# Kernel optimization log

Hardware: AMD Instinct MI355X
Metric: run time of the kernel (lower is better)

## Reference

```python
import jax, jax.numpy as jnp
import numpy as np

N, D, M, E, K = 16384, 512, 1024, 8, 2
LOSS_COEF = 0.01
EPS = 1e-10


def setup_inputs() -> dict:
    key = jax.random.key(0)
    ks = jax.random.split(key, 6)
    x = jax.random.normal(ks[0], (N, D), dtype=jnp.float32)
    # gate weight (torch init is zeros; use small random so routing is non-degenerate)
    w_gate = 0.02 * jax.random.normal(ks[1], (D, E), dtype=jnp.float32)
    # stacked expert FFN params: Linear(D->M), GELU, Linear(M->D)
    W1 = jax.random.normal(ks[2], (E, D, M), dtype=jnp.float32) / np.sqrt(D)
    b1 = jnp.zeros((E, M), dtype=jnp.float32)
    W2 = jax.random.normal(ks[3], (E, M, D), dtype=jnp.float32) / np.sqrt(M)
    b2 = jnp.zeros((E, D), dtype=jnp.float32)
    return {"x": x, "w_gate": w_gate, "W1": W1, "b1": b1, "W2": W2, "b2": b2}


def _cv_squared(v):
    # torch .var() is unbiased (ddof=1)
    v = v.astype(jnp.float32)
    return jnp.var(v, ddof=1) / (jnp.mean(v) ** 2 + EPS)


def reference(x, w_gate, W1, b1, W2, b2):
    n = x.shape[0]
    # --- noisy_top_k_gating (eval path: no noise) ---
    logits = x @ w_gate                                  # [N, E]
    top_logits, top_idx = jax.lax.top_k(logits, min(K + 1, E))
    topk_logits = top_logits[:, :K]                      # [N, K]
    topk_idx = top_idx[:, :K]                            # [N, K]
    topk_gates = jax.nn.softmax(topk_logits, axis=-1)    # [N, K]
    gates = jnp.zeros_like(logits).at[jnp.arange(n)[:, None], topk_idx].set(topk_gates)
    importance = gates.sum(axis=0)                       # [E]
    load = (gates > 0).sum(axis=0).astype(jnp.float32)   # [E]
    loss = LOSS_COEF * (_cv_squared(importance) + _cv_squared(load))
    # --- experts (dense equivalent of sparse dispatch/combine: gate==0 rows contribute 0) ---
    h = jnp.einsum('nd,edm->enm', x, W1) + b1[:, None, :]     # [E, N, M]
    h = jax.nn.gelu(h, approximate=False)
    out = jnp.einsum('enm,emd->end', h, W2) + b2[:, None, :]  # [E, N, D]
    y = jnp.einsum('ne,end->nd', gates, out)                  # [N, D]
    return (y, loss)
```

## Files before the change

kernel.cpp:

```cpp
#include <hip/hip_runtime.h>
#include <math.h>

#define NTOK 16384
#define DDIM 512
#define MDIM 1024
#define NEXP 8
#define BKW 32
#define TMAX 264

typedef __attribute__((ext_vector_type(8))) short short8;
typedef __attribute__((ext_vector_type(4))) float floatx4;

__device__ inline unsigned short f2bf(float f){
  union { float f; unsigned int u; } v; v.f = f;
  unsigned int u = v.u;
  u += ((u >> 16) & 1u) + 0x7fffu;
  return (unsigned short)(u >> 16);
}

__device__ inline float bf2f(unsigned short s){
  union { unsigned int u; float f; } v;
  v.u = ((unsigned int)s) << 16;
  return v.f;
}

__device__ inline float gelu_fast(float x){
  float u = x * 0.70710678118654752f;
  float a = fabsf(u);
  float t = __builtin_amdgcn_rcpf(fmaf(0.3275911f, a, 1.0f));
  float p = fmaf(1.061405429f, t, -1.453152027f);
  p = fmaf(p, t, 1.421413741f);
  p = fmaf(p, t, -0.284496736f);
  p = fmaf(p, t, 0.254829592f);
  p = p * t;
  float e = __expf(-u * u);
  float erfa = fmaf(-p, e, 1.0f);
  float erfu = copysignf(erfa, u);
  return 0.5f * x * (1.0f + erfu);
}

__device__ __forceinline__ void gload16(const unsigned short* g, unsigned short* l){
  __builtin_amdgcn_global_load_lds(
      (const __attribute__((address_space(1))) void*)g,
      (__attribute__((address_space(3))) void*)l,
      16, 0, 0);
}


__global__ void prep_kernel(const float* __restrict__ W1, const float* __restrict__ W2,
                            unsigned short* __restrict__ w1t, unsigned short* __restrict__ w2t,
                            int* __restrict__ counts, float* __restrict__ imp,
                            int* __restrict__ rank){
  __shared__ float tile[32][33];
  int z = blockIdx.z;
  if (z == 0 && blockIdx.x == 0 && blockIdx.y == 0){
    int flat = threadIdx.y * 32 + threadIdx.x;
    if (flat < NEXP){ counts[flat] = 0; imp[flat] = 0.0f; rank[flat] = 0; }
  }
  const float* in; unsigned short* out; int R, C, c0, r0, e;
  if (z < 8){ e = z;     in = W1; out = w1t; R = DDIM; C = MDIM; c0 = blockIdx.x << 5; r0 = blockIdx.y << 5; }
  else      { e = z - 8; in = W2; out = w2t; R = MDIM; C = DDIM; c0 = blockIdx.y << 5; r0 = blockIdx.x << 5; }
  const float* src = in + (size_t)e * R * C;
  unsigned short* dst = out + (size_t)e * R * C;
  int tc = threadIdx.x;
  int tr = threadIdx.y;
  #pragma unroll
  for (int i = 0; i < 32; i += 8)
    tile[tr + i][tc] = src[(size_t)(r0 + tr + i) * C + c0 + tc];
  __syncthreads();
  #pragma unroll
  for (int i = 0; i < 32; i += 8)
    dst[(size_t)(c0 + tr + i) * R + r0 + tc] = f2bf(tile[tc][tr + i]);
}


__global__ __launch_bounds__(256)
void gating_kernel(const float* __restrict__ x,
                   const float* __restrict__ wg,
                   unsigned short* __restrict__ xb,
                   int* __restrict__ tok_e, float* __restrict__ tok_g,
                   int* __restrict__ counts, float* __restrict__ imp){
  __shared__ int   lcnt[NEXP];
  __shared__ float limp[NEXP];
  int t = threadIdx.x;
  if (t < NEXP){ lcnt[t] = 0; limp[t] = 0.0f; }
  __syncthreads();

  int wave = t >> 6;
  int lane = t & 63;

  for (int it = 0; it < 4; it++){
    int n = blockIdx.x * 16 + it * 4 + wave;

    const float4* xp = (const float4*)(x + (size_t)n * DDIM + lane * 8);
    float4 a = xp[0], b = xp[1];
    float xv[8] = {a.x, a.y, a.z, a.w, b.x, b.y, b.z, b.w};

    short8 xo;
    #pragma unroll
    for (int j = 0; j < 8; j++) xo[j] = (short)f2bf(xv[j]);
    *(short8*)(xb + (size_t)n * DDIM + lane * 8) = xo;

    double acc[NEXP];
    #pragma unroll
    for (int e = 0; e < NEXP; e++) acc[e] = 0.0;
    #pragma unroll
    for (int j = 0; j < 8; j++){
      const float* wr = wg + (size_t)(lane * 8 + j) * NEXP;
      #pragma unroll
      for (int e = 0; e < NEXP; e++) acc[e] += (double)xv[j] * (double)wr[e];
    }
    #pragma unroll
    for (int off = 32; off >= 1; off >>= 1){
      #pragma unroll
      for (int e = 0; e < NEXP; e++) acc[e] += __shfl_xor(acc[e], off);
    }
    if (lane == 0){
      int i0 = -1, i1 = -1;
      double l0 = -1e300, l1 = -1e300;
      #pragma unroll
      for (int e = 0; e < NEXP; e++){
        double v = acc[e];
        if (v > l0){ l1 = l0; i1 = i0; l0 = v; i0 = e; }
        else if (v > l1){ l1 = v; i1 = e; }
      }
      float ex = expf((float)(l1 - l0));
      float g0 = 1.0f / (1.0f + ex);
      float g1 = ex / (1.0f + ex);
      tok_e[n * 2]     = i0; tok_e[n * 2 + 1] = i1;
      tok_g[n * 2]     = g0; tok_g[n * 2 + 1] = g1;
      atomicAdd(&lcnt[i0], 1); atomicAdd(&lcnt[i1], 1);
      atomicAdd(&limp[i0], g0); atomicAdd(&limp[i1], g1);
    }
  }
  __syncthreads();
  if (t < NEXP){
    atomicAdd(&counts[t], lcnt[t]);
    atomicAdd(&imp[t], limp[t]);
  }
}


__global__ __launch_bounds__(256)
void scatter_kernel(const int* __restrict__ counts,
                    const float* __restrict__ imp,
                    const int* __restrict__ tok_e,
                    const float* __restrict__ tok_g,
                    int* __restrict__ rank,
                    int* __restrict__ offsets_g, int* __restrict__ tile_pre_g,
                    int* __restrict__ btok, int* __restrict__ slot_of,
                    float* __restrict__ out_loss){
  __shared__ int lcnt[NEXP];
  __shared__ int lbase[NEXP];
  int t = threadIdx.x;
  if (t < NEXP) lcnt[t] = 0;
  __syncthreads();

  int n = blockIdx.x * 256 + t;
  int e0 = tok_e[n * 2], e1 = tok_e[n * 2 + 1];
  int r0 = atomicAdd(&lcnt[e0], 1);
  int r1 = atomicAdd(&lcnt[e1], 1);
  __syncthreads();
  if (t < NEXP){
    int offacc = 0;
    #pragma unroll
    for (int e = 0; e < NEXP; e++){ int c = counts[e]; if (e < t) offacc += c; }
    lbase[t] = offacc + atomicAdd(&rank[t], lcnt[t]);
  }
  __syncthreads();
  int s0 = lbase[e0] + r0;
  int s1 = lbase[e1] + r1;
  btok[s0] = n;
  btok[s1] = n;
  slot_of[n * 2]     = s0;
  slot_of[n * 2 + 1] = s1;

  if (blockIdx.x == 0 && t < 64){
    int l = t;
    int   c  = (l < NEXP) ? counts[l] : 0;
    float im = (l < NEXP) ? imp[l]    : 0.0f;
    int   tl = (c + 127) >> 7;
    int poff = 0, ptl = 0, tot = 0, tott = 0;
    double si = 0, si2 = 0, sl = 0, sl2 = 0;
    #pragma unroll
    for (int e = 0; e < NEXP; e++){
      int   ce = __shfl(c, e);
      int   te = __shfl(tl, e);
      float ie = __shfl(im, e);
      if (e < l){ poff += ce; ptl += te; }
      tot += ce; tott += te;
      si += (double)ie; si2 += (double)ie * ie;
      sl += (double)ce; sl2 += (double)ce * ce;
    }
    if (l < NEXP){ offsets_g[l] = poff; tile_pre_g[l] = ptl; }
    if (l == 0){
      offsets_g[NEXP] = tot; tile_pre_g[NEXP] = tott;
      double mi = si / 8.0, ml = sl / 8.0;
      double vi = (si2 - 8.0 * mi * mi) / 7.0;
      double vl = (sl2 - 8.0 * ml * ml) / 7.0;
      *out_loss = (float)(0.01 * (vi / (mi * mi + 1e-10) + vl / (ml * ml + 1e-10)));
    }
  }
}


__global__ __launch_bounds__(512, 6)
void gemm1_kernel(const unsigned short* __restrict__ xb,
                  const unsigned short* __restrict__ w1t,
                  const float* __restrict__ b1,
                  const int* __restrict__ offsets,
                  const int* __restrict__ tile_pre,
                  const int* __restrict__ btok,
                  unsigned short* __restrict__ H){
  int b = blockIdx.x;
  int L = (b & 7) * TMAX + (b >> 3);
  int ct = L & 7;
  int tt = L >> 3;
  if (tt >= tile_pre[NEXP]) return;
  int e = 0;
  while (tt >= tile_pre[e + 1]) e++;
  int rt = tt - tile_pre[e];
  int off = offsets[e];
  int cnt = offsets[e + 1] - off;
  int r0 = rt << 7;

  __shared__ unsigned short As[3 * 128 * BKW];
  __shared__ unsigned short Bs[3 * 128 * BKW];

  int t = threadIdx.x;
  int w = t >> 6;
  int l = t & 63;
  int g = (l & 3) ^ ((l >> 3) & 3);

  const unsigned short* apt;
  {
    int ra = r0 + w * 16 + (l >> 2);  if (ra >= cnt) ra = cnt - 1;
    apt = xb + (size_t)btok[off + ra] * DDIM + g * 8;
  }
  const unsigned short* bpt = w1t + ((size_t)e * MDIM + (ct << 7) + w * 16 + (l >> 2)) * DDIM + g * 8;

  int wr = (w >> 1) << 5;
  int wc = (w & 1) << 6;
  int lm = l & 15;
  int lq = l >> 4;
  int swz = (lm >> 1) & 3;

  int aoff[2], boff[4];
  #pragma unroll
  for (int i = 0; i < 2; i++) aoff[i] = (wr + i * 16 + lm) * BKW + ((lq ^ swz) << 3);
  #pragma unroll
  for (int j = 0; j < 4; j++) boff[j] = (wc + j * 16 + lm) * BKW + ((lq ^ swz) << 3);

  floatx4 acc[2][4] = {};

  #define STAGE1(K0, CB) {                                   \
    gload16(apt + (K0), As + (CB) * 4096 + w * 512);         \
    gload16(bpt + (K0), Bs + (CB) * 4096 + w * 512);         \
  }
  #define READ1(CB) {                                        \
    const unsigned short* Ac = As + (CB) * 4096;             \
    const unsigned short* Bc = Bs + (CB) * 4096;             \
    _Pragma("unroll")                                        \
    for (int i = 0; i < 2; i++) af[i]  = *(const short8*)(Ac + aoff[i]); \
    _Pragma("unroll")                                        \
    for (int j = 0; j < 4; j++) bfr[j] = *(const short8*)(Bc + boff[j]); \
  }
  #define MFMA1 {                                            \
    _Pragma("unroll")                                        \
    for (int i = 0; i < 2; i++)                              \
      _Pragma("unroll")                                      \
      for (int j = 0; j < 4; j++)                            \
        acc[i][j] = __builtin_amdgcn_mfma_f32_16x16x32_bf16(af[i], bfr[j], acc[i][j], 0, 0, 0); \
  }
  #define WAITBAR(N) {                                       \
    asm volatile("s_waitcnt vmcnt(" #N ")" ::: "memory");    \
    __builtin_amdgcn_sched_barrier(0);                       \
    __builtin_amdgcn_s_barrier();                            \
    __builtin_amdgcn_sched_barrier(0);                       \
  }

  const int NK = DDIM / BKW;
  STAGE1(0, 0);
  STAGE1(BKW, 1);
  WAITBAR(2);
  #pragma unroll
  for (int k = 0; k < NK; k++){
    const int cur = k % 3;
    short8 af[2], bfr[4];
    READ1(cur);
    if (k < NK - 2) STAGE1((k + 2) * BKW, (k + 2) % 3);
    __builtin_amdgcn_s_setprio(1);
    MFMA1;
    __builtin_amdgcn_s_setprio(0);
    if (k < NK - 2){ WAITBAR(2); }
    else if (k == NK - 2){ WAITBAR(0); }
  }
  #undef STAGE1
  #undef READ1
  #undef MFMA1
  #undef WAITBAR

  const float* bias = b1 + e * MDIM + (ct << 7);
  #pragma unroll
  for (int i = 0; i < 2; i++){
    int rbase = wr + i * 16 + lq * 4;
    #pragma unroll
    for (int j = 0; j < 4; j++){
      int cc = wc + j * 16 + lm;
      float bv = bias[cc];
      #pragma unroll
      for (int r = 0; r < 4; r++){
        int row = r0 + rbase + r;
        if (row < cnt){
          float v = acc[i][j][r] + bv;
          H[(size_t)(off + row) * MDIM + (ct << 7) + cc] = f2bf(gelu_fast(v));
        }
      }
    }
  }
}

__global__ __launch_bounds__(512, 6)
void gemm2_kernel(const unsigned short* __restrict__ H,
                  const unsigned short* __restrict__ w2t,
                  const float* __restrict__ b2,
                  const int* __restrict__ offsets,
                  const int* __restrict__ tile_pre,
                  unsigned short* __restrict__ O){
  int b = blockIdx.x;
  int L = (b & 7) * (TMAX / 2) + (b >> 3);
  int ct = L & 3;
  int tt = L >> 2;
  if (tt >= tile_pre[NEXP]) return;
  int e = 0;
  while (tt >= tile_pre[e + 1]) e++;
  int rt = tt - tile_pre[e];
  int off = offsets[e];
  int cnt = offsets[e + 1] - off;
  int r0 = rt << 7;

  __shared__ unsigned short As[3 * 128 * BKW];
  __shared__ unsigned short Bs[3 * 128 * BKW];

  int t = threadIdx.x;
  int w = t >> 6;
  int l = t & 63;
  int g = (l & 3) ^ ((l >> 3) & 3);

  const unsigned short* apt;
  {
    int ra = r0 + w * 16 + (l >> 2);  if (ra >= cnt) ra = cnt - 1;
    apt = H + (size_t)(off + ra) * MDIM + g * 8;
  }
  const unsigned short* bpt = w2t + ((size_t)e * DDIM + (ct << 7) + w * 16 + (l >> 2)) * MDIM + g * 8;

  int wr = (w >> 1) << 5;
  int wc = (w & 1) << 6;
  int lm = l & 15;
  int lq = l >> 4;
  int swz = (lm >> 1) & 3;

  int aoff[2], boff[4];
  #pragma unroll
  for (int i = 0; i < 2; i++) aoff[i] = (wr + i * 16 + lm) * BKW + ((lq ^ swz) << 3);
  #pragma unroll
  for (int j = 0; j < 4; j++) boff[j] = (wc + j * 16 + lm) * BKW + ((lq ^ swz) << 3);

  floatx4 acc[2][4] = {};

  #define STAGE2(K0, CB) {                                   \
    gload16(apt + (K0), As + (CB) * 4096 + w * 512);         \
    gload16(bpt + (K0), Bs + (CB) * 4096 + w * 512);         \
  }
  #define READ2(CB) {                                        \
    const unsigned short* Ac = As + (CB) * 4096;             \
    const unsigned short* Bc = Bs + (CB) * 4096;             \
    _Pragma("unroll")                                        \
    for (int i = 0; i < 2; i++) af[i]  = *(const short8*)(Ac + aoff[i]); \
    _Pragma("unroll")                                        \
    for (int j = 0; j < 4; j++) bfr[j] = *(const short8*)(Bc + boff[j]); \
  }
  #define MFMA2 {                                            \
    _Pragma("unroll")                                        \
    for (int i = 0; i < 2; i++)                              \
      _Pragma("unroll")                                      \
      for (int j = 0; j < 4; j++)                            \
        acc[i][j] = __builtin_amdgcn_mfma_f32_16x16x32_bf16(af[i], bfr[j], acc[i][j], 0, 0, 0); \
  }
  #define WAITBAR2(N) {                                      \
    asm volatile("s_waitcnt vmcnt(" #N ")" ::: "memory");    \
    __builtin_amdgcn_sched_barrier(0);                       \
    __builtin_amdgcn_s_barrier();                            \
    __builtin_amdgcn_sched_barrier(0);                       \
  }

  const int NK = MDIM / BKW;
  STAGE2(0, 0);
  STAGE2(BKW, 1);
  WAITBAR2(2);
  #pragma unroll
  for (int k = 0; k < NK; k++){
    const int cur = k % 3;
    short8 af[2], bfr[4];
    READ2(cur);
    if (k < NK - 2) STAGE2((k + 2) * BKW, (k + 2) % 3);
    __builtin_amdgcn_s_setprio(1);
    MFMA2;
    __builtin_amdgcn_s_setprio(0);
    if (k < NK - 2){ WAITBAR2(2); }
    else if (k == NK - 2){ WAITBAR2(0); }
  }
  #undef STAGE2
  #undef READ2
  #undef MFMA2
  #undef WAITBAR2

  const float* bias = b2 + e * DDIM + (ct << 7);
  #pragma unroll
  for (int i = 0; i < 2; i++){
    int rbase = wr + i * 16 + lq * 4;
    #pragma unroll
    for (int j = 0; j < 4; j++){
      int cc = wc + j * 16 + lm;
      float bv = bias[cc];
      #pragma unroll
      for (int r = 0; r < 4; r++){
        int row = r0 + rbase + r;
        if (row < cnt)
          O[(size_t)(off + row) * DDIM + (ct << 7) + cc] = f2bf(acc[i][j][r] + bv);
      }
    }
  }
}


__global__ __launch_bounds__(256)
void combine_kernel(const unsigned short* __restrict__ O,
                    const float* __restrict__ tok_g,
                    const int* __restrict__ slot_of,
                    float* __restrict__ y){
  int wave = threadIdx.x >> 6;
  int lane = threadIdx.x & 63;
  int n = blockIdx.x * 4 + wave;
  int s0 = slot_of[n * 2], s1 = slot_of[n * 2 + 1];
  float g0 = tok_g[n * 2], g1 = tok_g[n * 2 + 1];
  short8 a = *(const short8*)(O + (size_t)s0 * DDIM + lane * 8);
  short8 b = *(const short8*)(O + (size_t)s1 * DDIM + lane * 8);
  float4 o0, o1;
  float* po0 = (float*)&o0;
  float* po1 = (float*)&o1;
  #pragma unroll
  for (int j = 0; j < 4; j++){
    po0[j] = g0 * bf2f((unsigned short)a[j]) + g1 * bf2f((unsigned short)b[j]);
    po1[j] = g0 * bf2f((unsigned short)a[j + 4]) + g1 * bf2f((unsigned short)b[j + 4]);
  }
  float4* yp = (float4*)(y + (size_t)n * DDIM + lane * 8);
  yp[0] = o0;
  yp[1] = o1;
}


extern "C" void kernel_launch(void* const* d_in, const int* in_sizes, int n_in,
                              void* d_out, int out_size, void* d_ws, size_t ws_size,
                              hipStream_t stream){
  const float* x  = (const float*)d_in[0];
  const float* wg = (const float*)d_in[1];
  const float* W1 = (const float*)d_in[2];
  const float* b1 = (const float*)d_in[3];
  const float* W2 = (const float*)d_in[4];
  const float* b2 = (const float*)d_in[5];
  float* y = (float*)d_out;

  char* ws = (char*)d_ws;
  size_t o = 0;
  auto alloc = [&](size_t bytes)->char*{
    char* p = ws + o;
    o += (bytes + 255) & ~(size_t)255;
    return p;
  };
  unsigned short* xb   = (unsigned short*)alloc((size_t)NTOK * DDIM * 2);
  unsigned short* w1t  = (unsigned short*)alloc((size_t)NEXP * MDIM * DDIM * 2);
  unsigned short* w2t  = (unsigned short*)alloc((size_t)NEXP * DDIM * MDIM * 2);
  unsigned short* H    = (unsigned short*)alloc((size_t)NTOK * 2 * MDIM * 2);
  unsigned short* O    = (unsigned short*)alloc((size_t)NTOK * 2 * DDIM * 2);
  int*   btok    = (int*)  alloc((size_t)NTOK * 2 * 4);
  int*   slot_of = (int*)  alloc((size_t)NTOK * 2 * 4);
  int*   tok_e   = (int*)  alloc((size_t)NTOK * 2 * 4);
  float* tok_g   = (float*)alloc((size_t)NTOK * 2 * 4);
  int*   counts  = (int*)  alloc(64);
  float* imp     = (float*)alloc(64);
  int*   rank    = (int*)  alloc(64);
  int*   offsets = (int*)  alloc(64);
  int*   tile_pre= (int*)  alloc(64);

  hipLaunchKernelGGL(prep_kernel, dim3(32, 16, 16), dim3(32, 8), 0, stream,
                     W1, W2, w1t, w2t, counts, imp, rank);
  hipLaunchKernelGGL(gating_kernel, dim3(NTOK / 16), dim3(256), 0, stream,
                     x, wg, xb, tok_e, tok_g, counts, imp);
  hipLaunchKernelGGL(scatter_kernel, dim3(NTOK / 256), dim3(256), 0, stream,
                     counts, imp, tok_e, tok_g, rank, offsets, tile_pre,
                     btok, slot_of, y + (size_t)NTOK * DDIM);
  hipLaunchKernelGGL(gemm1_kernel, dim3(TMAX * 8), dim3(512), 0, stream,
                     xb, w1t, b1, offsets, tile_pre, btok, H);
  hipLaunchKernelGGL(gemm2_kernel, dim3(TMAX * 4), dim3(512), 0, stream,
                     H, w2t, b2, offsets, tile_pre, O);
  hipLaunchKernelGGL(combine_kernel, dim3(NTOK / 4), dim3(256), 0, stream,
                     O, tok_g, slot_of, y);
}
```

Baseline: 268.3 us.

## Fuse weight prep into gating kernel and scatter GEMM2 outputs to token order

```diff
diff --git a/kernel.cpp b/kernel.cpp
--- a/kernel.cpp
+++ b/kernel.cpp
@@ -47,42 +47,39 @@
 }
 
 
-__global__ void prep_kernel(const float* __restrict__ W1, const float* __restrict__ W2,
-                            unsigned short* __restrict__ w1t, unsigned short* __restrict__ w2t,
-                            int* __restrict__ counts, float* __restrict__ imp,
-                            int* __restrict__ rank){
+__global__ __launch_bounds__(256)
+void prep_gating_kernel(const float* __restrict__ x,
+                        const float* __restrict__ wg,
+                        const float* __restrict__ W1, const float* __restrict__ W2,
+                        unsigned short* __restrict__ xb,
+                        unsigned short* __restrict__ w1t, unsigned short* __restrict__ w2t,
+                        int* __restrict__ tok_e, float* __restrict__ tok_g,
+                        int* __restrict__ counts, float* __restrict__ imp){
   __shared__ float tile[32][33];
-  int z = blockIdx.z;
-  if (z == 0 && blockIdx.x == 0 && blockIdx.y == 0){
-    int flat = threadIdx.y * 32 + threadIdx.x;
-    if (flat < NEXP){ counts[flat] = 0; imp[flat] = 0.0f; rank[flat] = 0; }
-  }
-  const float* in; unsigned short* out; int R, C, c0, r0, e;
-  if (z < 8){ e = z;     in = W1; out = w1t; R = DDIM; C = MDIM; c0 = blockIdx.x << 5; r0 = blockIdx.y << 5; }
-  else      { e = z - 8; in = W2; out = w2t; R = MDIM; C = DDIM; c0 = blockIdx.y << 5; r0 = blockIdx.x << 5; }
-  const float* src = in + (size_t)e * R * C;
-  unsigned short* dst = out + (size_t)e * R * C;
-  int tc = threadIdx.x;
-  int tr = threadIdx.y;
-  #pragma unroll
-  for (int i = 0; i < 32; i += 8)
-    tile[tr + i][tc] = src[(size_t)(r0 + tr + i) * C + c0 + tc];
-  __syncthreads();
-  #pragma unroll
-  for (int i = 0; i < 32; i += 8)
-    dst[(size_t)(c0 + tr + i) * R + r0 + tc] = f2bf(tile[tc][tr + i]);
-}
-
-
-__global__ __launch_bounds__(256)
-void gating_kernel(const float* __restrict__ x,
-                   const float* __restrict__ wg,
-                   unsigned short* __restrict__ xb,
-                   int* __restrict__ tok_e, float* __restrict__ tok_g,
-                   int* __restrict__ counts, float* __restrict__ imp){
   __shared__ int   lcnt[NEXP];
   __shared__ float limp[NEXP];
   int t = threadIdx.x;
+
+  if (blockIdx.x >= 1024){
+    int pb = blockIdx.x - 1024;
+    int bx = pb & 31, by = (pb >> 5) & 15, z = pb >> 9;
+    const float* in; unsigned short* out; int R, C, c0, r0, e;
+    if (z < 8){ e = z;     in = W1; out = w1t; R = DDIM; C = MDIM; c0 = bx << 5; r0 = by << 5; }
+    else      { e = z - 8; in = W2; out = w2t; R = MDIM; C = DDIM; c0 = by << 5; r0 = bx << 5; }
+    const float* src = in + (size_t)e * R * C;
+    unsigned short* dst = out + (size_t)e * R * C;
+    int tc = t & 31;
+    int tr = t >> 5;
+    #pragma unroll
+    for (int i = 0; i < 32; i += 8)
+      tile[tr + i][tc] = src[(size_t)(r0 + tr + i) * C + c0 + tc];
+    __syncthreads();
+    #pragma unroll
+    for (int i = 0; i < 32; i += 8)
+      dst[(size_t)(c0 + tr + i) * R + r0 + tc] = f2bf(tile[tc][tr + i]);
+    return;
+  }
+
   if (t < NEXP){ lcnt[t] = 0; limp[t] = 0.0f; }
   __syncthreads();
 
@@ -145,10 +142,9 @@
 void scatter_kernel(const int* __restrict__ counts,
                     const float* __restrict__ imp,
                     const int* __restrict__ tok_e,
-                    const float* __restrict__ tok_g,
                     int* __restrict__ rank,
                     int* __restrict__ offsets_g, int* __restrict__ tile_pre_g,
-                    int* __restrict__ btok, int* __restrict__ slot_of,
+                    int* __restrict__ btok, int* __restrict__ slot_tok2,
                     float* __restrict__ out_loss){
   __shared__ int lcnt[NEXP];
   __shared__ int lbase[NEXP];
@@ -172,8 +168,8 @@
   int s1 = lbase[e1] + r1;
   btok[s0] = n;
   btok[s1] = n;
-  slot_of[n * 2]     = s0;
-  slot_of[n * 2 + 1] = s1;
+  slot_tok2[s0] = n * 2;
+  slot_tok2[s1] = n * 2 + 1;
 
   if (blockIdx.x == 0 && t < 64){
     int l = t;
@@ -326,6 +322,7 @@
                   const float* __restrict__ b2,
                   const int* __restrict__ offsets,
                   const int* __restrict__ tile_pre,
+                  const int* __restrict__ slot_tok2,
                   unsigned short* __restrict__ O){
   int b = blockIdx.x;
   int L = (b & 7) * (TMAX / 2) + (b >> 3);
@@ -420,14 +417,15 @@
   for (int i = 0; i < 2; i++){
     int rbase = wr + i * 16 + lq * 4;
     #pragma unroll
-    for (int j = 0; j < 4; j++){
-      int cc = wc + j * 16 + lm;
-      float bv = bias[cc];
-      #pragma unroll
-      for (int r = 0; r < 4; r++){
-        int row = r0 + rbase + r;
-        if (row < cnt)
-          O[(size_t)(off + row) * DDIM + (ct << 7) + cc] = f2bf(acc[i][j][r] + bv);
+    for (int r = 0; r < 4; r++){
+      int row = r0 + rbase + r;
+      if (row < cnt){
+        int t2 = slot_tok2[off + row];
+        #pragma unroll
+        for (int j = 0; j < 4; j++){
+          int cc = wc + j * 16 + lm;
+          O[(size_t)t2 * DDIM + (ct << 7) + cc] = f2bf(acc[i][j][r] + bias[cc]);
+        }
       }
     }
   }
@@ -437,15 +435,13 @@
 __global__ __launch_bounds__(256)
 void combine_kernel(const unsigned short* __restrict__ O,
                     const float* __restrict__ tok_g,
-                    const int* __restrict__ slot_of,
                     float* __restrict__ y){
   int wave = threadIdx.x >> 6;
   int lane = threadIdx.x & 63;
   int n = blockIdx.x * 4 + wave;
-  int s0 = slot_of[n * 2], s1 = slot_of[n * 2 + 1];
   float g0 = tok_g[n * 2], g1 = tok_g[n * 2 + 1];
-  short8 a = *(const short8*)(O + (size_t)s0 * DDIM + lane * 8);
-  short8 b = *(const short8*)(O + (size_t)s1 * DDIM + lane * 8);
+  short8 a = *(const short8*)(O + (size_t)(n * 2)     * DDIM + lane * 8);
+  short8 b = *(const short8*)(O + (size_t)(n * 2 + 1) * DDIM + lane * 8);
   float4 o0, o1;
   float* po0 = (float*)&o0;
   float* po1 = (float*)&o1;
@@ -483,27 +479,26 @@
   unsigned short* w2t  = (unsigned short*)alloc((size_t)NEXP * DDIM * MDIM * 2);
   unsigned short* H    = (unsigned short*)alloc((size_t)NTOK * 2 * MDIM * 2);
   unsigned short* O    = (unsigned short*)alloc((size_t)NTOK * 2 * DDIM * 2);
-  int*   btok    = (int*)  alloc((size_t)NTOK * 2 * 4);
-  int*   slot_of = (int*)  alloc((size_t)NTOK * 2 * 4);
-  int*   tok_e   = (int*)  alloc((size_t)NTOK * 2 * 4);
-  float* tok_g   = (float*)alloc((size_t)NTOK * 2 * 4);
-  int*   counts  = (int*)  alloc(64);
-  float* imp     = (float*)alloc(64);
-  int*   rank    = (int*)  alloc(64);
-  int*   offsets = (int*)  alloc(64);
-  int*   tile_pre= (int*)  alloc(64);
-
-  hipLaunchKernelGGL(prep_kernel, dim3(32, 16, 16), dim3(32, 8), 0, stream,
-                     W1, W2, w1t, w2t, counts, imp, rank);
-  hipLaunchKernelGGL(gating_kernel, dim3(NTOK / 16), dim3(256), 0, stream,
-                     x, wg, xb, tok_e, tok_g, counts, imp);
+  int*   btok     = (int*)  alloc((size_t)NTOK * 2 * 4);
+  int*   slot_tok2= (int*)  alloc((size_t)NTOK * 2 * 4);
+  int*   tok_e    = (int*)  alloc((size_t)NTOK * 2 * 4);
+  float* tok_g    = (float*)alloc((size_t)NTOK * 2 * 4);
+  int*   counts   = (int*)  alloc(64);
+  float* imp      = (float*)alloc(64);
+  int*   rank     = (int*)  alloc(64);
+  int*   offsets  = (int*)  alloc(64);
+  int*   tile_pre = (int*)  alloc(64);
+
+  hipMemsetAsync(counts, 0, 768, stream);
+  hipLaunchKernelGGL(prep_gating_kernel, dim3(1024 + 8192), dim3(256), 0, stream,
+                     x, wg, W1, W2, xb, w1t, w2t, tok_e, tok_g, counts, imp);
   hipLaunchKernelGGL(scatter_kernel, dim3(NTOK / 256), dim3(256), 0, stream,
-                     counts, imp, tok_e, tok_g, rank, offsets, tile_pre,
-                     btok, slot_of, y + (size_t)NTOK * DDIM);
+                     counts, imp, tok_e, rank, offsets, tile_pre,
+                     btok, slot_tok2, y + (size_t)NTOK * DDIM);
   hipLaunchKernelGGL(gemm1_kernel, dim3(TMAX * 8), dim3(512), 0, stream,
                      xb, w1t, b1, offsets, tile_pre, btok, H);
   hipLaunchKernelGGL(gemm2_kernel, dim3(TMAX * 4), dim3(512), 0, stream,
-                     H, w2t, b2, offsets, tile_pre, O);
+                     H, w2t, b2, offsets, tile_pre, slot_tok2, O);
   hipLaunchKernelGGL(combine_kernel, dim3(NTOK / 4), dim3(256), 0, stream,
-                     O, tok_g, slot_of, y);
-}
+                     O, tok_g, y);
+}
```

Measured after the change: 271.5 us. No clear change (+1.2%).
